# Kernel tuning notes

Measured on AMD Instinct MI355X. Metric: run time of the kernel, lower is better.

The kernel has to match this reference:

```python
import jax, jax.numpy as jnp
import numpy as np

D_EMBED = 1024
D_HIDDEN = 1024
BATCH = 8192


def setup_inputs() -> dict:
    key = jax.random.key(0)
    ks = jax.random.split(key, 11)
    din = D_EMBED + D_HIDDEN
    s = 1.0 / np.sqrt(din)  # torch Linear default init scale
    def lin(kw, kb):
        W = jax.random.uniform(kw, (din, D_HIDDEN), minval=-s, maxval=s, dtype=jnp.float32)
        b = jax.random.uniform(kb, (D_HIDDEN,), minval=-s, maxval=s, dtype=jnp.float32)
        return W, b
    Wf, bf = lin(ks[0], ks[1])
    Wi, bi = lin(ks[2], ks[3])
    Wo, bo = lin(ks[4], ks[5])
    Wu, bu = lin(ks[6], ks[7])
    x = jax.random.normal(ks[8], (BATCH, D_EMBED), dtype=jnp.float32)
    h = jax.random.normal(ks[9], (BATCH, D_HIDDEN), dtype=jnp.float32)
    c = jax.random.normal(ks[10], (BATCH, D_HIDDEN), dtype=jnp.float32)
    return {"x": x, "h": h, "c": c,
            "Wf": Wf, "bf": bf, "Wi": Wi, "bi": bi,
            "Wo": Wo, "bo": bo, "Wu": Wu, "bu": bu}


def reference(x, h, c, Wf, bf, Wi, bi, Wo, bo, Wu, bu):
    xh = jnp.concatenate([x, h], axis=-1)              # [B, d_embed+d_hidden]
    # Fused gate GEMM: concat weights along output dim -> one [B, 4H] matmul.
    W = jnp.concatenate([Wf, Wi, Wo, Wu], axis=1)      # [din, 4H]
    b = jnp.concatenate([bf, bi, bo, bu], axis=0)      # [4H]
    gates = xh @ W + b                                 # [B, 4H]
    f, i, o, u = jnp.split(gates, 4, axis=-1)
    f = jax.nn.sigmoid(f)
    i = jax.nn.sigmoid(i)
    o = jax.nn.sigmoid(o)
    c_hat = jnp.tanh(u)
    new_c = f * c + i * c_hat
    new_h = o * jnp.tanh(new_c)
    return (new_h, new_c)
```

## Files before the change

kernel.cpp:

```cpp
#include <hip/hip_runtime.h>
#include <hip/hip_bf16.h>

#define BATCH 8192
#define DK    2048
#define DH    1024
#define DN    4096

typedef __attribute__((ext_vector_type(8))) short bf16x8;
typedef __attribute__((ext_vector_type(4))) short short4v;
typedef __attribute__((ext_vector_type(4))) float f32x4;

__device__ __forceinline__ unsigned short f2bf(float f) {
    union { float f; unsigned u; } v; v.f = f;
    unsigned r = v.u + 0x7FFFu + ((v.u >> 16) & 1u);
    return (unsigned short)(r >> 16);
}
__device__ __forceinline__ float bf2f(unsigned short b) {
    union { unsigned u; float f; } v; v.u = ((unsigned)b) << 16; return v.f;
}
__device__ __forceinline__ float sigm(float x)  { return 1.0f / (1.0f + __expf(-x)); }
__device__ __forceinline__ float tanh_(float x) { return 1.0f - 2.0f / (1.0f + __expf(2.0f * x)); }

__device__ __forceinline__ void glds16(const void* g, void* l) {
    __builtin_amdgcn_global_load_lds(
        (const __attribute__((address_space(1))) unsigned*)g,
        (__attribute__((address_space(3))) unsigned*)l, 16, 0, 0);
}

__global__ void cvtA_k(const float* __restrict__ x, const float* __restrict__ h,
                       short* __restrict__ A) {
    long t = (long)blockIdx.x * 256 + threadIdx.x;
    long idx = t << 3;
    long b   = idx >> 10;
    int  col = (int)(idx & 1023);
    {
        float4 v0 = *(const float4*)(x + idx);
        float4 v1 = *(const float4*)(x + idx + 4);
        bf16x8 s;
        s[0]=(short)f2bf(v0.x); s[1]=(short)f2bf(v0.y); s[2]=(short)f2bf(v0.z); s[3]=(short)f2bf(v0.w);
        s[4]=(short)f2bf(v1.x); s[5]=(short)f2bf(v1.y); s[6]=(short)f2bf(v1.z); s[7]=(short)f2bf(v1.w);
        *(bf16x8*)(A + b * DK + col) = s;
    }
    {
        float4 v0 = *(const float4*)(h + idx);
        float4 v1 = *(const float4*)(h + idx + 4);
        bf16x8 s;
        s[0]=(short)f2bf(v0.x); s[1]=(short)f2bf(v0.y); s[2]=(short)f2bf(v0.z); s[3]=(short)f2bf(v0.w);
        s[4]=(short)f2bf(v1.x); s[5]=(short)f2bf(v1.y); s[6]=(short)f2bf(v1.z); s[7]=(short)f2bf(v1.w);
        *(bf16x8*)(A + b * DK + 1024 + col) = s;
    }
}

__global__ void cvtW_k(const float* __restrict__ Wg, short* __restrict__ Wt) {
    __shared__ float tile[64][65];
    int k0 = blockIdx.x << 6;
    int j0 = blockIdx.y << 6;
    int tid = threadIdx.x;
    int rr = tid >> 4, c4 = (tid & 15) << 2;
#pragma unroll
    for (int i = 0; i < 4; i++) {
        int r = rr + (i << 4);
        float4 v = *(const float4*)(Wg + (long)(k0 + r) * DH + j0 + c4);
        tile[r][c4] = v.x; tile[r][c4+1] = v.y; tile[r][c4+2] = v.z; tile[r][c4+3] = v.w;
    }
    __syncthreads();
#pragma unroll
    for (int i = 0; i < 4; i++) {
        int jr = rr + (i << 4);
        short4v s;
        s[0]=(short)f2bf(tile[c4+0][jr]); s[1]=(short)f2bf(tile[c4+1][jr]);
        s[2]=(short)f2bf(tile[c4+2][jr]); s[3]=(short)f2bf(tile[c4+3][jr]);
        *(short4v*)(Wt + (long)(j0 + jr) * DK + k0 + c4) = s;
    }
}

__launch_bounds__(256, 2)
__global__ void gemm_k(const short* __restrict__ A, const short* __restrict__ W,
                       short* __restrict__ G) {
    __shared__ short sA[2][4096];
    __shared__ short sB[2][4096];

    int bid = blockIdx.x;
    int wg  = ((bid & 7) << 8) + (bid >> 3);
    int nt  = wg >> 6;
    int mt  = wg & 63;
    int tid = threadIdx.x;
    int lane = tid & 63;
    int wv = tid >> 6, wr = wv >> 1, wc = wv & 1;

    long baseA[2], baseB[2];
    int  ldso[2];
#pragma unroll
    for (int c = 0; c < 2; c++) {
        int r  = (c << 6) + (tid >> 2);
        int s  = tid & 3;
        int ss = s ^ ((r ^ (r >> 2)) & 3);
        baseA[c] = (long)(mt * 128 + r) * DK + ss * 8;
        baseB[c] = (long)(nt * 128 + r) * DK + ss * 8;
        ldso[c]  = (c << 12) + (tid << 4);
    }

    int offA[4], offB[4];
#pragma unroll
    for (int i = 0; i < 4; i++) {
        int rA = (wr << 6) + (i << 4) + (lane & 15);
        offA[i] = (rA << 6) + ((((lane >> 4)) ^ ((rA ^ (rA >> 2)) & 3)) << 4);
        int rB = (wc << 6) + (i << 4) + (lane & 15);
        offB[i] = (rB << 6) + ((((lane >> 4)) ^ ((rB ^ (rB >> 2)) & 3)) << 4);
    }

    f32x4 acc[4][4];
    const f32x4 fz = {0.f, 0.f, 0.f, 0.f};
#pragma unroll
    for (int i = 0; i < 4; i++)
#pragma unroll
        for (int j = 0; j < 4; j++) acc[i][j] = fz;

    auto STAGE = [&](int buf, int kt) {
        const short* a0 = A + (long)kt * 32;
        const short* b0 = W + (long)kt * 32;
        char* la = (char*)&sA[buf][0];
        char* lb = (char*)&sB[buf][0];
#pragma unroll
        for (int c = 0; c < 2; c++) {
            glds16(a0 + baseA[c], la + ldso[c]);
            glds16(b0 + baseB[c], lb + ldso[c]);
        }
    };
    auto COMPUTE = [&](int buf) {
        const char* la = (const char*)&sA[buf][0];
        const char* lb = (const char*)&sB[buf][0];
        bf16x8 av[4], bv[4];
#pragma unroll
        for (int i = 0; i < 4; i++) {
            av[i] = *(const bf16x8*)(la + offA[i]);
            bv[i] = *(const bf16x8*)(lb + offB[i]);
        }
#pragma unroll
        for (int i = 0; i < 4; i++)
#pragma unroll
            for (int j = 0; j < 4; j++)
                acc[i][j] = __builtin_amdgcn_mfma_f32_16x16x32_bf16(av[i], bv[j], acc[i][j], 0, 0, 0);
    };

    STAGE(0, 0);
    __syncthreads();
    int cur = 0;
    for (int kt = 1; kt < DK / 32; ++kt) {
        STAGE(cur ^ 1, kt);
        COMPUTE(cur);
        __syncthreads();
        cur ^= 1;
    }
    COMPUTE(cur);

    long row0 = (long)mt * 128 + (wr << 6) + ((lane >> 4) << 2);
    int  col0 = nt * 128 + (wc << 6) + (lane & 15);
#pragma unroll
    for (int i = 0; i < 4; i++)
#pragma unroll
        for (int j = 0; j < 4; j++) {
            long r = row0 + (i << 4);
            int  cc = col0 + (j << 4);
#pragma unroll
            for (int q = 0; q < 4; q++)
                G[(r + q) * DN + cc] = (short)f2bf(acc[i][j][q]);
        }
}

__global__ void ep_k(const short* __restrict__ G, const float* __restrict__ cin,
                     const float* __restrict__ bfv, const float* __restrict__ biv,
                     const float* __restrict__ bov, const float* __restrict__ buv,
                     float* __restrict__ out) {
    long t = (long)blockIdx.x * 256 + threadIdx.x;
    long idx = t << 3;
    long b   = idx >> 10;
    int  col = (int)(idx & 1023);
    long gb  = b << 12;

    bf16x8 fg = *(const bf16x8*)(G + gb + col);
    bf16x8 ig = *(const bf16x8*)(G + gb + 1024 + col);
    bf16x8 og = *(const bf16x8*)(G + gb + 2048 + col);
    bf16x8 ug = *(const bf16x8*)(G + gb + 3072 + col);

    float4 c0 = *(const float4*)(cin + idx), c1 = *(const float4*)(cin + idx + 4);
    float4 f0 = *(const float4*)(bfv + col), f1 = *(const float4*)(bfv + col + 4);
    float4 i0 = *(const float4*)(biv + col), i1 = *(const float4*)(biv + col + 4);
    float4 o0 = *(const float4*)(bov + col), o1 = *(const float4*)(bov + col + 4);
    float4 u0 = *(const float4*)(buv + col), u1 = *(const float4*)(buv + col + 4);

    float cv[8] = {c0.x,c0.y,c0.z,c0.w,c1.x,c1.y,c1.z,c1.w};
    float ba[8] = {f0.x,f0.y,f0.z,f0.w,f1.x,f1.y,f1.z,f1.w};
    float bb[8] = {i0.x,i0.y,i0.z,i0.w,i1.x,i1.y,i1.z,i1.w};
    float bc[8] = {o0.x,o0.y,o0.z,o0.w,o1.x,o1.y,o1.z,o1.w};
    float bd[8] = {u0.x,u0.y,u0.z,u0.w,u1.x,u1.y,u1.z,u1.w};

    float hv[8], ncv[8];
#pragma unroll
    for (int q = 0; q < 8; q++) {
        float f  = sigm(bf2f((unsigned short)fg[q]) + ba[q]);
        float i_ = sigm(bf2f((unsigned short)ig[q]) + bb[q]);
        float o_ = sigm(bf2f((unsigned short)og[q]) + bc[q]);
        float u_ = tanh_(bf2f((unsigned short)ug[q]) + bd[q]);
        float nc = f * cv[q] + i_ * u_;
        ncv[q] = nc;
        hv[q]  = o_ * tanh_(nc);
    }
    float4 h0 = {hv[0],hv[1],hv[2],hv[3]},  h1 = {hv[4],hv[5],hv[6],hv[7]};
    float4 n0 = {ncv[0],ncv[1],ncv[2],ncv[3]}, n1 = {ncv[4],ncv[5],ncv[6],ncv[7]};
    *(float4*)(out + idx)     = h0;
    *(float4*)(out + idx + 4) = h1;
    *(float4*)(out + (long)BATCH * DH + idx)     = n0;
    *(float4*)(out + (long)BATCH * DH + idx + 4) = n1;
}

__global__ void naive_k(const float* __restrict__ x, const float* __restrict__ h,
                        const float* __restrict__ cin,
                        const float* __restrict__ Wf, const float* __restrict__ bfv,
                        const float* __restrict__ Wi, const float* __restrict__ biv,
                        const float* __restrict__ Wo, const float* __restrict__ bov,
                        const float* __restrict__ Wu, const float* __restrict__ buv,
                        float* __restrict__ out) {
    long t = (long)blockIdx.x * 256 + threadIdx.x;
    long b = t >> 10; int j = (int)(t & 1023);
    float sf = bfv[j], si = biv[j], so = bov[j], su = buv[j];
    for (int k = 0; k < 1024; k++) {
        float xv = x[b * 1024 + k];
        long w = (long)k * 1024 + j;
        sf += xv * Wf[w]; si += xv * Wi[w]; so += xv * Wo[w]; su += xv * Wu[w];
    }
    for (int k = 0; k < 1024; k++) {
        float hv = h[b * 1024 + k];
        long w = (long)(k + 1024) * 1024 + j;
        sf += hv * Wf[w]; si += hv * Wi[w]; so += hv * Wo[w]; su += hv * Wu[w];
    }
    float f = sigm(sf), i_ = sigm(si), o_ = sigm(so), u_ = tanh_(su);
    float nc = f * cin[t] + i_ * u_;
    out[t] = o_ * tanh_(nc);
    out[(long)BATCH * DH + t] = nc;
}

extern "C" void kernel_launch(void* const* d_in, const int* in_sizes, int n_in,
                              void* d_out, int out_size, void* d_ws, size_t ws_size,
                              hipStream_t stream) {
    const float* x   = (const float*)d_in[0];
    const float* h   = (const float*)d_in[1];
    const float* c   = (const float*)d_in[2];
    const float* Wf  = (const float*)d_in[3];
    const float* bf_ = (const float*)d_in[4];
    const float* Wi  = (const float*)d_in[5];
    const float* bi_ = (const float*)d_in[6];
    const float* Wo  = (const float*)d_in[7];
    const float* bo_ = (const float*)d_in[8];
    const float* Wu  = (const float*)d_in[9];
    const float* bu_ = (const float*)d_in[10];
    float* out = (float*)d_out;

    const size_t needA = (size_t)BATCH * DK * 2;
    const size_t needW = (size_t)DN * DK * 2;
    const size_t needG = (size_t)BATCH * DN * 2;

    if (ws_size < needA + needW + needG) {
        naive_k<<<(BATCH * DH) / 256, 256, 0, stream>>>(x, h, c, Wf, bf_, Wi, bi_, Wo, bo_, Wu, bu_, out);
        return;
    }

    short* Abf = (short*)d_ws;
    short* Wt  = (short*)((char*)d_ws + needA);
    short* G   = (short*)((char*)d_ws + needA + needW);

    cvtA_k<<<(BATCH * DH) / (256 * 8), 256, 0, stream>>>(x, h, Abf);
    dim3 tg(DK / 64, DH / 64);
    cvtW_k<<<tg, 256, 0, stream>>>(Wf, Wt + 0L * DH * DK / 1024 * 1024);
    cvtW_k<<<tg, 256, 0, stream>>>(Wi, Wt + 1L * DH * DK);
    cvtW_k<<<tg, 256, 0, stream>>>(Wo, Wt + 2L * DH * DK);
    cvtW_k<<<tg, 256, 0, stream>>>(Wu, Wt + 3L * DH * DK);
    gemm_k<<<(BATCH / 128) * (DN / 128), 256, 0, stream>>>(Abf, Wt, G);
    ep_k<<<(BATCH * DH) / (256 * 8), 256, 0, stream>>>(G, c, bf_, bi_, bo_, bu_, out);
}
```

Before: 384.2 us.

## Fuse LSTM epilogue into GEMM with interleaved gate weights and 256x256 tiles

Weights are interleaved per 16 hidden units across the four gates, so each GEMM workgroup holds all four gate values for the same hidden columns and applies the LSTM epilogue in registers. This removes the bf16 gate intermediate buffer and the separate epilogue kernel. The GEMM moves to 256x256 tiles with 512 threads, a 4-stage LDS pipeline using explicit vmcnt waits, and s_setprio around the MFMA blocks. The four weight-conversion launches are merged into one. In exchange the epilogue does scattered scalar loads and stores of c and the outputs, and the 128KB LDS footprint limits occupancy to one workgroup per CU.

```diff
diff --git a/kernel.cpp b/kernel.cpp
--- a/kernel.cpp
+++ b/kernel.cpp
@@ -5,6 +5,7 @@
 #define DK    2048
 #define DH    1024
 #define DN    4096
+#define NT    64
 
 typedef __attribute__((ext_vector_type(8))) short bf16x8;
 typedef __attribute__((ext_vector_type(4))) short short4v;
@@ -14,9 +15,6 @@
     union { float f; unsigned u; } v; v.f = f;
     unsigned r = v.u + 0x7FFFu + ((v.u >> 16) & 1u);
     return (unsigned short)(r >> 16);
-}
-__device__ __forceinline__ float bf2f(unsigned short b) {
-    union { unsigned u; float f; } v; v.u = ((unsigned)b) << 16; return v.f;
 }
 __device__ __forceinline__ float sigm(float x)  { return 1.0f / (1.0f + __expf(-x)); }
 __device__ __forceinline__ float tanh_(float x) { return 1.0f - 2.0f / (1.0f + __expf(2.0f * x)); }
@@ -51,8 +49,12 @@
     }
 }
 
-__global__ void cvtW_k(const float* __restrict__ Wg, short* __restrict__ Wt) {
+__global__ void cvtW_k(const float* __restrict__ W0, const float* __restrict__ W1,
+                       const float* __restrict__ W2, const float* __restrict__ W3,
+                       short* __restrict__ Wt) {
     __shared__ float tile[64][65];
+    const int g = blockIdx.z;
+    const float* Wg = (g == 0) ? W0 : (g == 1) ? W1 : (g == 2) ? W2 : W3;
     int k0 = blockIdx.x << 6;
     int j0 = blockIdx.y << 6;
     int tid = threadIdx.x;
@@ -67,151 +69,128 @@
 #pragma unroll
     for (int i = 0; i < 4; i++) {
         int jr = rr + (i << 4);
+        int j  = j0 + jr;
+        int n  = ((j >> 4) << 6) + (g << 4) + (j & 15);
         short4v s;
         s[0]=(short)f2bf(tile[c4+0][jr]); s[1]=(short)f2bf(tile[c4+1][jr]);
         s[2]=(short)f2bf(tile[c4+2][jr]); s[3]=(short)f2bf(tile[c4+3][jr]);
-        *(short4v*)(Wt + (long)(j0 + jr) * DK + k0 + c4) = s;
-    }
-}
-
-__launch_bounds__(256, 2)
+        *(short4v*)(Wt + (long)n * DK + k0 + c4) = s;
+    }
+}
+
+__launch_bounds__(512, 1)
 __global__ void gemm_k(const short* __restrict__ A, const short* __restrict__ W,
-                       short* __restrict__ G) {
-    __shared__ short sA[2][4096];
-    __shared__ short sB[2][4096];
-
-    int bid = blockIdx.x;
-    int wg  = ((bid & 7) << 8) + (bid >> 3);
-    int nt  = wg >> 6;
-    int mt  = wg & 63;
-    int tid = threadIdx.x;
-    int lane = tid & 63;
-    int wv = tid >> 6, wr = wv >> 1, wc = wv & 1;
-
-    long baseA[2], baseB[2];
-    int  ldso[2];
-#pragma unroll
-    for (int c = 0; c < 2; c++) {
-        int r  = (c << 6) + (tid >> 2);
-        int s  = tid & 3;
-        int ss = s ^ ((r ^ (r >> 2)) & 3);
-        baseA[c] = (long)(mt * 128 + r) * DK + ss * 8;
-        baseB[c] = (long)(nt * 128 + r) * DK + ss * 8;
-        ldso[c]  = (c << 12) + (tid << 4);
-    }
-
-    int offA[4], offB[4];
-#pragma unroll
-    for (int i = 0; i < 4; i++) {
-        int rA = (wr << 6) + (i << 4) + (lane & 15);
-        offA[i] = (rA << 6) + ((((lane >> 4)) ^ ((rA ^ (rA >> 2)) & 3)) << 4);
-        int rB = (wc << 6) + (i << 4) + (lane & 15);
-        offB[i] = (rB << 6) + ((((lane >> 4)) ^ ((rB ^ (rB >> 2)) & 3)) << 4);
-    }
-
-    f32x4 acc[4][4];
+                       const float* __restrict__ cin,
+                       const float* __restrict__ bfv, const float* __restrict__ biv,
+                       const float* __restrict__ bov, const float* __restrict__ buv,
+                       float* __restrict__ out) {
+    __shared__ char sA[65536];
+    __shared__ char sB[65536];
+
+    const int bid = blockIdx.x;
+    const int wg  = ((bid & 7) << 6) + (bid >> 3);
+    const int nt  = wg >> 5;
+    const int mt  = wg & 31;
+    const int tid = threadIdx.x;
+    const int lane = tid & 63;
+    const int wv = tid >> 6;
+    const int wr = wv >> 2;
+    const int wc = wv & 3;
+
+    const int srow  = tid >> 2;
+    const int sslot = (tid & 3) ^ ((tid >> 3) & 3);
+    const long a0 = (long)(mt * 256 + srow)       * DK + sslot * 8;
+    const long a1 = (long)(mt * 256 + 128 + srow) * DK + sslot * 8;
+    const long b0 = (long)(nt * 256 + srow)       * DK + sslot * 8;
+    const long b1 = (long)(nt * 256 + 128 + srow) * DK + sslot * 8;
+
+    int offA[8], offB[4];
+#pragma unroll
+    for (int i = 0; i < 8; i++) {
+        int rA = (wr << 7) + (i << 4) + (lane & 15);
+        offA[i] = (rA << 6) + (((lane >> 4) ^ ((rA >> 1) & 3)) << 4);
+    }
+#pragma unroll
+    for (int g = 0; g < 4; g++) {
+        int rB = (wc << 6) + (g << 4) + (lane & 15);
+        offB[g] = (rB << 6) + (((lane >> 4) ^ ((rB >> 1) & 3)) << 4);
+    }
+
+    f32x4 acc[8][4];
     const f32x4 fz = {0.f, 0.f, 0.f, 0.f};
 #pragma unroll
-    for (int i = 0; i < 4; i++)
-#pragma unroll
-        for (int j = 0; j < 4; j++) acc[i][j] = fz;
-
-    auto STAGE = [&](int buf, int kt) {
-        const short* a0 = A + (long)kt * 32;
-        const short* b0 = W + (long)kt * 32;
-        char* la = (char*)&sA[buf][0];
-        char* lb = (char*)&sB[buf][0];
-#pragma unroll
-        for (int c = 0; c < 2; c++) {
-            glds16(a0 + baseA[c], la + ldso[c]);
-            glds16(b0 + baseB[c], lb + ldso[c]);
+    for (int i = 0; i < 8; i++)
+#pragma unroll
+        for (int g = 0; g < 4; g++) acc[i][g] = fz;
+
+    auto STAGE = [&](int t) {
+        const int buf = t & 3;
+        char* la = sA + (buf << 14) + (tid << 4);
+        char* lb = sB + (buf << 14) + (tid << 4);
+        const long ko = (long)t << 5;
+        glds16(A + a0 + ko, la);
+        glds16(A + a1 + ko, la + 8192);
+        glds16(W + b0 + ko, lb);
+        glds16(W + b1 + ko, lb + 8192);
+    };
+
+    auto BODY = [&](int t, bool doStage, int vml) {
+        const int bo2 = (t & 3) << 14;
+        if (doStage) STAGE(t + 3);
+        bf16x8 bv[4], av[4];
+#pragma unroll
+        for (int g = 0; g < 4; g++) bv[g] = *(const bf16x8*)(sB + bo2 + offB[g]);
+#pragma unroll
+        for (int i = 0; i < 4; i++) av[i] = *(const bf16x8*)(sA + bo2 + offA[i]);
+        __builtin_amdgcn_s_setprio(1);
+#pragma unroll
+        for (int i = 0; i < 4; i++)
+#pragma unroll
+            for (int g = 0; g < 4; g++)
+                acc[i][g] = __builtin_amdgcn_mfma_f32_16x16x32_bf16(av[i], bv[g], acc[i][g], 0, 0, 0);
+        __builtin_amdgcn_s_setprio(0);
+#pragma unroll
+        for (int i = 0; i < 4; i++) av[i] = *(const bf16x8*)(sA + bo2 + offA[i + 4]);
+        __builtin_amdgcn_s_setprio(1);
+#pragma unroll
+        for (int i = 0; i < 4; i++)
+#pragma unroll
+            for (int g = 0; g < 4; g++)
+                acc[i + 4][g] = __builtin_amdgcn_mfma_f32_16x16x32_bf16(av[i], bv[g], acc[i + 4][g], 0, 0, 0);
+        __builtin_amdgcn_s_setprio(0);
+        if (vml == 8)      asm volatile("s_waitcnt vmcnt(8)" ::: "memory");
+        else if (vml == 4) asm volatile("s_waitcnt vmcnt(4)" ::: "memory");
+        else if (vml == 0) asm volatile("s_waitcnt vmcnt(0)" ::: "memory");
+        if (vml >= 0) __builtin_amdgcn_s_barrier();
+    };
+
+    STAGE(0); STAGE(1); STAGE(2);
+    asm volatile("s_waitcnt vmcnt(8)" ::: "memory");
+    __builtin_amdgcn_s_barrier();
+
+#pragma unroll 1
+    for (int t = 0; t <= NT - 4; ++t) BODY(t, true, 8);
+    BODY(NT - 3, false, 4);
+    BODY(NT - 2, false, 0);
+    BODY(NT - 1, false, -1);
+
+    const int hid = nt * 64 + wc * 16 + (lane & 15);
+    const long rowb = (long)mt * 256 + (wr << 7) + ((lane >> 4) << 2);
+    const float b_f = bfv[hid], b_i = biv[hid], b_o = bov[hid], b_u = buv[hid];
+#pragma unroll
+    for (int i = 0; i < 8; i++) {
+#pragma unroll
+        for (int q = 0; q < 4; q++) {
+            const long r = rowb + (i << 4) + q;
+            float f  = sigm(acc[i][0][q] + b_f);
+            float i_ = sigm(acc[i][1][q] + b_i);
+            float o_ = sigm(acc[i][2][q] + b_o);
+            float u_ = tanh_(acc[i][3][q] + b_u);
+            float nc = f * cin[r * DH + hid] + i_ * u_;
+            out[r * DH + hid] = o_ * tanh_(nc);
+            out[(long)BATCH * DH + r * DH + hid] = nc;
         }
-    };
-    auto COMPUTE = [&](int buf) {
-        const char* la = (const char*)&sA[buf][0];
-        const char* lb = (const char*)&sB[buf][0];
-        bf16x8 av[4], bv[4];
-#pragma unroll
-        for (int i = 0; i < 4; i++) {
-            av[i] = *(const bf16x8*)(la + offA[i]);
-            bv[i] = *(const bf16x8*)(lb + offB[i]);
-        }
-#pragma unroll
-        for (int i = 0; i < 4; i++)
-#pragma unroll
-            for (int j = 0; j < 4; j++)
-                acc[i][j] = __builtin_amdgcn_mfma_f32_16x16x32_bf16(av[i], bv[j], acc[i][j], 0, 0, 0);
-    };
-
-    STAGE(0, 0);
-    __syncthreads();
-    int cur = 0;
-    for (int kt = 1; kt < DK / 32; ++kt) {
-        STAGE(cur ^ 1, kt);
-        COMPUTE(cur);
-        __syncthreads();
-        cur ^= 1;
-    }
-    COMPUTE(cur);
-
-    long row0 = (long)mt * 128 + (wr << 6) + ((lane >> 4) << 2);
-    int  col0 = nt * 128 + (wc << 6) + (lane & 15);
-#pragma unroll
-    for (int i = 0; i < 4; i++)
-#pragma unroll
-        for (int j = 0; j < 4; j++) {
-            long r = row0 + (i << 4);
-            int  cc = col0 + (j << 4);
-#pragma unroll
-            for (int q = 0; q < 4; q++)
-                G[(r + q) * DN + cc] = (short)f2bf(acc[i][j][q]);
-        }
-}
-
-__global__ void ep_k(const short* __restrict__ G, const float* __restrict__ cin,
-                     const float* __restrict__ bfv, const float* __restrict__ biv,
-                     const float* __restrict__ bov, const float* __restrict__ buv,
-                     float* __restrict__ out) {
-    long t = (long)blockIdx.x * 256 + threadIdx.x;
-    long idx = t << 3;
-    long b   = idx >> 10;
-    int  col = (int)(idx & 1023);
-    long gb  = b << 12;
-
-    bf16x8 fg = *(const bf16x8*)(G + gb + col);
-    bf16x8 ig = *(const bf16x8*)(G + gb + 1024 + col);
-    bf16x8 og = *(const bf16x8*)(G + gb + 2048 + col);
-    bf16x8 ug = *(const bf16x8*)(G + gb + 3072 + col);
-
-    float4 c0 = *(const float4*)(cin + idx), c1 = *(const float4*)(cin + idx + 4);
-    float4 f0 = *(const float4*)(bfv + col), f1 = *(const float4*)(bfv + col + 4);
-    float4 i0 = *(const float4*)(biv + col), i1 = *(const float4*)(biv + col + 4);
-    float4 o0 = *(const float4*)(bov + col), o1 = *(const float4*)(bov + col + 4);
-    float4 u0 = *(const float4*)(buv + col), u1 = *(const float4*)(buv + col + 4);
-
-    float cv[8] = {c0.x,c0.y,c0.z,c0.w,c1.x,c1.y,c1.z,c1.w};
-    float ba[8] = {f0.x,f0.y,f0.z,f0.w,f1.x,f1.y,f1.z,f1.w};
-    float bb[8] = {i0.x,i0.y,i0.z,i0.w,i1.x,i1.y,i1.z,i1.w};
-    float bc[8] = {o0.x,o0.y,o0.z,o0.w,o1.x,o1.y,o1.z,o1.w};
-    float bd[8] = {u0.x,u0.y,u0.z,u0.w,u1.x,u1.y,u1.z,u1.w};
-
-    float hv[8], ncv[8];
-#pragma unroll
-    for (int q = 0; q < 8; q++) {
-        float f  = sigm(bf2f((unsigned short)fg[q]) + ba[q]);
-        float i_ = sigm(bf2f((unsigned short)ig[q]) + bb[q]);
-        float o_ = sigm(bf2f((unsigned short)og[q]) + bc[q]);
-        float u_ = tanh_(bf2f((unsigned short)ug[q]) + bd[q]);
-        float nc = f * cv[q] + i_ * u_;
-        ncv[q] = nc;
-        hv[q]  = o_ * tanh_(nc);
-    }
-    float4 h0 = {hv[0],hv[1],hv[2],hv[3]},  h1 = {hv[4],hv[5],hv[6],hv[7]};
-    float4 n0 = {ncv[0],ncv[1],ncv[2],ncv[3]}, n1 = {ncv[4],ncv[5],ncv[6],ncv[7]};
-    *(float4*)(out + idx)     = h0;
-    *(float4*)(out + idx + 4) = h1;
-    *(float4*)(out + (long)BATCH * DH + idx)     = n0;
-    *(float4*)(out + (long)BATCH * DH + idx + 4) = n1;
+    }
 }
 
 __global__ void naive_k(const float* __restrict__ x, const float* __restrict__ h,
@@ -258,23 +237,16 @@
 
     const size_t needA = (size_t)BATCH * DK * 2;
     const size_t needW = (size_t)DN * DK * 2;
-    const size_t needG = (size_t)BATCH * DN * 2;
-
-    if (ws_size < needA + needW + needG) {
+
+    if (ws_size < needA + needW) {
         naive_k<<<(BATCH * DH) / 256, 256, 0, stream>>>(x, h, c, Wf, bf_, Wi, bi_, Wo, bo_, Wu, bu_, out);
         return;
     }
 
     short* Abf = (short*)d_ws;
     short* Wt  = (short*)((char*)d_ws + needA);
-    short* G   = (short*)((char*)d_ws + needA + needW);
 
     cvtA_k<<<(BATCH * DH) / (256 * 8), 256, 0, stream>>>(x, h, Abf);
-    dim3 tg(DK / 64, DH / 64);
-    cvtW_k<<<tg, 256, 0, stream>>>(Wf, Wt + 0L * DH * DK / 1024 * 1024);
-    cvtW_k<<<tg, 256, 0, stream>>>(Wi, Wt + 1L * DH * DK);
-    cvtW_k<<<tg, 256, 0, stream>>>(Wo, Wt + 2L * DH * DK);
-    cvtW_k<<<tg, 256, 0, stream>>>(Wu, Wt + 3L * DH * DK);
-    gemm_k<<<(BATCH / 128) * (DN / 128), 256, 0, stream>>>(Abf, Wt, G);
-    ep_k<<<(BATCH * DH) / (256 * 8), 256, 0, stream>>>(G, c, bf_, bi_, bo_, bu_, out);
-}
+    cvtW_k<<<dim3(DK / 64, DH / 64, 4), 256, 0, stream>>>(Wf, Wi, Wo, Wu, Wt);
+    gemm_k<<<512, 512, 0, stream>>>(Abf, Wt, c, bf_, bi_, bo_, bu_, out);
+}
```

New measurement: 354.2 us. 1.08x faster.
